# Kernel optimization log

Hardware: AMD Instinct MI355X
Metric: run time of the kernel (lower is better)

## Reference

```python
import jax, jax.numpy as jnp
import numpy as np

NEG_SLOPE = 0.2  # PyG GATConv default


def gat_conv(x, W, a_src, a_dst, b, src, dst, n):
    """Single-head PyG-style GATConv with self-loops already appended to (src, dst)."""
    h = x @ W                                   # [N, F]
    alpha_src = h @ a_src                       # [N]
    alpha_dst = h @ a_dst                       # [N]
    e = alpha_src[src] + alpha_dst[dst]         # [E] per-edge logit (message j->i)
    e = jax.nn.leaky_relu(e, NEG_SLOPE)
    # numerically stable softmax over edges grouped by destination node
    m = jax.ops.segment_max(e, dst, num_segments=n)
    ex = jnp.exp(e - m[dst])
    denom = jax.ops.segment_sum(ex, dst, num_segments=n)
    alpha = ex / denom[dst]                     # [E]
    out = jax.ops.segment_sum(alpha[:, None] * h[src], dst, num_segments=n)
    return out + b


def setup_inputs() -> dict:
    key = jax.random.key(0)
    ks = jax.random.split(key, 16)
    N, C, E = 50000, 128, 800000
    x = jax.random.normal(ks[0], (N, C), dtype=jnp.float32)
    edge_index = jax.random.randint(ks[1], (2, E), 0, N, dtype=jnp.int64)

    def lin(k, din, dout):
        return jax.random.normal(k, (din, dout), dtype=jnp.float32) / np.sqrt(din)

    def att(k, d):
        return jax.random.normal(k, (d,), dtype=jnp.float32) / np.sqrt(d)

    d1, d2, d3 = 2 * C, C // 2, 1
    return {
        "x": x, "edge_index": edge_index,
        "W1": lin(ks[2], C, d1), "as1": att(ks[3], d1), "ad1": att(ks[4], d1), "b1": jnp.zeros((d1,), jnp.float32),
        "W2": lin(ks[5], d1, d2), "as2": att(ks[6], d2), "ad2": att(ks[7], d2), "b2": jnp.zeros((d2,), jnp.float32),
        "W3": lin(ks[8], d2, d3), "as3": att(ks[9], d3), "ad3": att(ks[10], d3), "b3": jnp.zeros((d3,), jnp.float32),
    }


def reference(x, edge_index, W1, as1, ad1, b1, W2, as2, ad2, b2, W3, as3, ad3, b3):
    n = x.shape[0]
    self_loops = jnp.arange(n, dtype=edge_index.dtype)
    src = jnp.concatenate([edge_index[0], self_loops])
    dst = jnp.concatenate([edge_index[1], self_loops])
    # dropout is identity in eval mode
    h = gat_conv(x, W1, as1, ad1, b1, src, dst, n)
    h = jax.nn.elu(h)
    h = gat_conv(h, W2, as2, ad2, b2, src, dst, n)
    h = jax.nn.elu(h)
    return gat_conv(h, W3, as3, ad3, b3, src, dst, n)
```

## Files before the change

### kernel.cpp

```cpp
#include <hip/hip_runtime.h>
#include <hip/hip_bf16.h>
#include <hip/hip_fp16.h>
#include <math.h>

#define NEG_SLOPE 0.2f

typedef __attribute__((ext_vector_type(8))) short bf16x8_t;
typedef __attribute__((ext_vector_type(4))) float f32x4_t;

struct __align__(8) half4_t { __half2 a, b; };

__global__ void hist_k(const int* __restrict__ ei, int E, int n, int* __restrict__ deg) {
    int e = blockIdx.x * 256 + threadIdx.x;
    int ET = E + n;
    if (e >= ET) return;
    int d = (e < E) ? ei[E + e] : (e - E);
    atomicAdd(&deg[d], 1);
}

__global__ void scan1_k(const int* __restrict__ deg, int* __restrict__ incl,
                        int* __restrict__ bsums, int n) {
    __shared__ int s[256];
    int tid = threadIdx.x;
    int i = blockIdx.x * 256 + tid;
    int v = (i < n) ? deg[i] : 0;
    s[tid] = v;
    __syncthreads();
    for (int off = 1; off < 256; off <<= 1) {
        int t = (tid >= off) ? s[tid - off] : 0;
        __syncthreads();
        s[tid] += t;
        __syncthreads();
    }
    if (i < n) incl[i] = s[tid];
    if (tid == 255) bsums[blockIdx.x] = s[255];
}

__global__ void scan2_k(int* __restrict__ bsums, int nch) {
    __shared__ int s[256];
    int tid = threadIdx.x;
    int v = (tid < nch) ? bsums[tid] : 0;
    int orig = v;
    s[tid] = v;
    __syncthreads();
    for (int off = 1; off < 256; off <<= 1) {
        int t = (tid >= off) ? s[tid - off] : 0;
        __syncthreads();
        s[tid] += t;
        __syncthreads();
    }
    if (tid < nch) bsums[tid] = s[tid] - orig;
}

__global__ void scan3_k(int* __restrict__ offsets, int* __restrict__ cursor,
                        const int* __restrict__ bsums, int n, int total) {
    int i = blockIdx.x * 256 + threadIdx.x;
    if (i < n) {
        int excl = offsets[i] - cursor[i] + bsums[i >> 8];
        offsets[i] = excl;
        cursor[i]  = excl;
    }
    if (i == 0 && blockIdx.x == 0) offsets[n] = total;
}

__global__ void fill_k(const int* __restrict__ ei, int E, int n,
                       int* __restrict__ cursor, int* __restrict__ csr) {
    int e = blockIdx.x * 256 + threadIdx.x;
    int ET = E + n;
    if (e >= ET) return;
    int s, d;
    if (e < E) { s = ei[e]; d = ei[E + e]; }
    else       { s = e - E; d = e - E; }
    int pos = atomicAdd(&cursor[d], 1);
    csr[pos] = s;
}

__device__ inline void bf16_split(float f, ushort& hi, ushort& lo) {
    unsigned int u = __float_as_uint(f);
    unsigned int r = u + 0x7FFFu + ((u >> 16) & 1u);
    hi = (ushort)(r >> 16);
    float back = __uint_as_float((unsigned int)hi << 16);
    float rem = f - back;
    unsigned int u2 = __float_as_uint(rem);
    unsigned int r2 = u2 + 0x7FFFu + ((u2 >> 16) & 1u);
    lo = (ushort)(r2 >> 16);
}

__global__ __launch_bounds__(256) void gemm_split_k(const float* __restrict__ A,
                                                    const float* __restrict__ B,
                                                    float* __restrict__ C,
                                                    __half* __restrict__ Ch,
                                                    int M, int K, int Nc) {
    __shared__ __align__(16) ushort sAh[128][40];
    __shared__ __align__(16) ushort sAl[128][40];
    __shared__ __align__(16) ushort sBh[64][40];
    __shared__ __align__(16) ushort sBl[64][40];

    const int tid  = threadIdx.x;
    const int lane = tid & 63;
    const int wv   = tid >> 6;
    const int wm   = wv & 1, wn = wv >> 1;
    const int m0   = blockIdx.x << 7;
    const int n0   = blockIdx.y << 6;

    f32x4_t acc[4][2];
#pragma unroll
    for (int i = 0; i < 4; i++)
#pragma unroll
        for (int j = 0; j < 2; j++) acc[i][j] = (f32x4_t){0.f, 0.f, 0.f, 0.f};

    const int arow = tid >> 1;
    const int acb  = (tid & 1) << 4;
    const int bcol = tid & 63;
    const int bkb  = (tid >> 6) << 3;

    for (int k0 = 0; k0 < K; k0 += 32) {
        {
            float fv[16];
            const int gr = m0 + arow;
            if (gr < M) {
                const float* ap = A + (size_t)gr * K + k0 + acb;
#pragma unroll
                for (int q = 0; q < 4; q++) {
                    float4 t = *(const float4*)(ap + (q << 2));
                    fv[q * 4 + 0] = t.x; fv[q * 4 + 1] = t.y;
                    fv[q * 4 + 2] = t.z; fv[q * 4 + 3] = t.w;
                }
            } else {
#pragma unroll
                for (int q = 0; q < 16; q++) fv[q] = 0.f;
            }
            ushort hv[16], lv[16];
#pragma unroll
            for (int q = 0; q < 16; q++) bf16_split(fv[q], hv[q], lv[q]);
            *(bf16x8_t*)&sAh[arow][acb]     = *(bf16x8_t*)&hv[0];
            *(bf16x8_t*)&sAh[arow][acb + 8] = *(bf16x8_t*)&hv[8];
            *(bf16x8_t*)&sAl[arow][acb]     = *(bf16x8_t*)&lv[0];
            *(bf16x8_t*)&sAl[arow][acb + 8] = *(bf16x8_t*)&lv[8];
        }
        {
            float fv[8];
#pragma unroll
            for (int j = 0; j < 8; j++)
                fv[j] = B[(size_t)(k0 + bkb + j) * Nc + n0 + bcol];
            ushort hv[8], lv[8];
#pragma unroll
            for (int j = 0; j < 8; j++) bf16_split(fv[j], hv[j], lv[j]);
            *(bf16x8_t*)&sBh[bcol][bkb] = *(bf16x8_t*)&hv[0];
            *(bf16x8_t*)&sBl[bcol][bkb] = *(bf16x8_t*)&lv[0];
        }
        __syncthreads();
        bf16x8_t ah[4], al[4], bh[2], bl[2];
        const int rbase = (wm << 6) + (lane & 15);
        const int slot  = (lane >> 4) << 3;
#pragma unroll
        for (int mi = 0; mi < 4; mi++) {
            ah[mi] = *(const bf16x8_t*)&sAh[rbase + (mi << 4)][slot];
            al[mi] = *(const bf16x8_t*)&sAl[rbase + (mi << 4)][slot];
        }
        const int cbase = (wn << 5) + (lane & 15);
#pragma unroll
        for (int ni = 0; ni < 2; ni++) {
            bh[ni] = *(const bf16x8_t*)&sBh[cbase + (ni << 4)][slot];
            bl[ni] = *(const bf16x8_t*)&sBl[cbase + (ni << 4)][slot];
        }
#pragma unroll
        for (int mi = 0; mi < 4; mi++)
#pragma unroll
            for (int ni = 0; ni < 2; ni++) {
                acc[mi][ni] = __builtin_amdgcn_mfma_f32_16x16x32_bf16(ah[mi], bh[ni], acc[mi][ni], 0, 0, 0);
                acc[mi][ni] = __builtin_amdgcn_mfma_f32_16x16x32_bf16(ah[mi], bl[ni], acc[mi][ni], 0, 0, 0);
                acc[mi][ni] = __builtin_amdgcn_mfma_f32_16x16x32_bf16(al[mi], bh[ni], acc[mi][ni], 0, 0, 0);
            }
        __syncthreads();
    }
#pragma unroll
    for (int mi = 0; mi < 4; mi++)
#pragma unroll
        for (int ni = 0; ni < 2; ni++) {
            int row = m0 + (wm << 6) + (mi << 4) + ((lane >> 4) << 2);
            int col = n0 + (wn << 5) + (ni << 4) + (lane & 15);
#pragma unroll
            for (int r = 0; r < 4; r++) {
                if (row + r < M) {
                    float v = acc[mi][ni][r];
                    C[(size_t)(row + r) * Nc + col]  = v;
                    Ch[(size_t)(row + r) * Nc + col] = __float2half(v);
                }
            }
        }
}

template <int D>
__global__ void prep_k(const float* __restrict__ h, const float* __restrict__ avs,
                       const float* __restrict__ avd, float* __restrict__ as_o,
                       float* __restrict__ ad_o, int n) {
    int wid = (blockIdx.x << 2) + (threadIdx.x >> 6);
    int lane = threadIdx.x & 63;
    if (wid >= n) return;
    const float* row = h + (size_t)wid * D;
    float s = 0.f, d = 0.f;
#pragma unroll
    for (int u = 0; u < D / 64; u++) {
        float hv = row[u * 64 + lane];
        s = fmaf(hv, avs[u * 64 + lane], s);
        d = fmaf(hv, avd[u * 64 + lane], d);
    }
#pragma unroll
    for (int o = 32; o; o >>= 1) {
        s += __shfl_xor(s, o);
        d += __shfl_xor(d, o);
    }
    if (lane == 0) { as_o[wid] = s; ad_o[wid] = d; }
}

#define DEG_CAP 128

template <int D, bool DO_ELU>
__global__ __launch_bounds__(256) void agg_k(const int* __restrict__ offs,
                                             const int* __restrict__ csr,
                                             const float* __restrict__ asb,
                                             const float* __restrict__ adb,
                                             const __half* __restrict__ h,
                                             const float* __restrict__ bias,
                                             float* __restrict__ out, int n) {
    __shared__ float wsh[4][DEG_CAP];
    __shared__ int   jsh[4][DEG_CAP];
    const int wv   = threadIdx.x >> 6;
    const int lane = threadIdx.x & 63;
    const int wid  = (blockIdx.x << 2) + wv;
    const bool active = wid < n;

    int beg = 0, deg = 0;
    float adi = 0.f;
    if (active) {
        beg = offs[wid];
        deg = offs[wid + 1] - beg;
        adi = adb[wid];
    }
    const int degc = deg < DEG_CAP ? deg : DEG_CAP;

    float m = -INFINITY;
    if (active) {
        for (int e = lane; e < degc; e += 64) {
            int j = csr[beg + e];
            float v = asb[j] + adi;
            v = v > 0.f ? v : NEG_SLOPE * v;
            jsh[wv][e] = j;
            wsh[wv][e] = v;
            m = fmaxf(m, v);
        }
        for (int e = DEG_CAP + lane; e < deg; e += 64) {
            float v = asb[csr[beg + e]] + adi;
            v = v > 0.f ? v : NEG_SLOPE * v;
            m = fmaxf(m, v);
        }
#pragma unroll
        for (int o = 32; o; o >>= 1) m = fmaxf(m, __shfl_xor(m, o));
    }

    float inv = 0.f;
    if (active) {
        float ssum = 0.f;
        for (int e = lane; e < degc; e += 64) {
            float ww = __expf(wsh[wv][e] - m);
            wsh[wv][e] = ww;
            ssum += ww;
        }
        for (int e = DEG_CAP + lane; e < deg; e += 64) {
            float v = asb[csr[beg + e]] + adi;
            v = v > 0.f ? v : NEG_SLOPE * v;
            ssum += __expf(v - m);
        }
#pragma unroll
        for (int o = 32; o; o >>= 1) ssum += __shfl_xor(ssum, o);
        inv = 1.f / ssum;
    }

    __syncthreads();

    if (!active) return;

    constexpr int U = D / 64;
    float a0[U] = {}, a1[U] = {}, a2[U] = {}, a3[U] = {};

    int e = 0;
    for (; e + 4 <= degc; e += 4) {
        int j0 = jsh[wv][e], j1 = jsh[wv][e + 1], j2 = jsh[wv][e + 2], j3 = jsh[wv][e + 3];
        float w0 = wsh[wv][e], w1 = wsh[wv][e + 1], w2 = wsh[wv][e + 2], w3 = wsh[wv][e + 3];
        if constexpr (U == 4) {
            const half4_t h0 = *(const half4_t*)(h + (size_t)j0 * D + (lane << 2));
            const half4_t h1 = *(const half4_t*)(h + (size_t)j1 * D + (lane << 2));
            const half4_t h2 = *(const half4_t*)(h + (size_t)j2 * D + (lane << 2));
            const half4_t h3 = *(const half4_t*)(h + (size_t)j3 * D + (lane << 2));
            float2 f0a = __half22float2(h0.a), f0b = __half22float2(h0.b);
            float2 f1a = __half22float2(h1.a), f1b = __half22float2(h1.b);
            float2 f2a = __half22float2(h2.a), f2b = __half22float2(h2.b);
            float2 f3a = __half22float2(h3.a), f3b = __half22float2(h3.b);
            a0[0] = fmaf(w0, f0a.x, a0[0]); a0[1] = fmaf(w0, f0a.y, a0[1]);
            a0[2] = fmaf(w0, f0b.x, a0[2]); a0[3] = fmaf(w0, f0b.y, a0[3]);
            a1[0] = fmaf(w1, f1a.x, a1[0]); a1[1] = fmaf(w1, f1a.y, a1[1]);
            a1[2] = fmaf(w1, f1b.x, a1[2]); a1[3] = fmaf(w1, f1b.y, a1[3]);
            a2[0] = fmaf(w2, f2a.x, a2[0]); a2[1] = fmaf(w2, f2a.y, a2[1]);
            a2[2] = fmaf(w2, f2b.x, a2[2]); a2[3] = fmaf(w2, f2b.y, a2[3]);
            a3[0] = fmaf(w3, f3a.x, a3[0]); a3[1] = fmaf(w3, f3a.y, a3[1]);
            a3[2] = fmaf(w3, f3b.x, a3[2]); a3[3] = fmaf(w3, f3b.y, a3[3]);
        } else {
            a0[0] = fmaf(w0, __half2float(h[(size_t)j0 * D + lane]), a0[0]);
            a1[0] = fmaf(w1, __half2float(h[(size_t)j1 * D + lane]), a1[0]);
            a2[0] = fmaf(w2, __half2float(h[(size_t)j2 * D + lane]), a2[0]);
            a3[0] = fmaf(w3, __half2float(h[(size_t)j3 * D + lane]), a3[0]);
        }
    }
    for (; e < degc; ++e) {
        int j = jsh[wv][e];
        float ww = wsh[wv][e];
        if constexpr (U == 4) {
            const half4_t hv = *(const half4_t*)(h + (size_t)j * D + (lane << 2));
            float2 fa = __half22float2(hv.a), fb = __half22float2(hv.b);
            a0[0] = fmaf(ww, fa.x, a0[0]); a0[1] = fmaf(ww, fa.y, a0[1]);
            a0[2] = fmaf(ww, fb.x, a0[2]); a0[3] = fmaf(ww, fb.y, a0[3]);
        } else {
            a0[0] = fmaf(ww, __half2float(h[(size_t)j * D + lane]), a0[0]);
        }
    }
    for (int eo = DEG_CAP; eo < deg; ++eo) {
        int j = csr[beg + eo];
        float v = asb[j] + adi;
        v = v > 0.f ? v : NEG_SLOPE * v;
        float ww = __expf(v - m);
        if constexpr (U == 4) {
            const half4_t hv = *(const half4_t*)(h + (size_t)j * D + (lane << 2));
            float2 fa = __half22float2(hv.a), fb = __half22float2(hv.b);
            a0[0] = fmaf(ww, fa.x, a0[0]); a0[1] = fmaf(ww, fa.y, a0[1]);
            a0[2] = fmaf(ww, fb.x, a0[2]); a0[3] = fmaf(ww, fb.y, a0[3]);
        } else {
            a0[0] = fmaf(ww, __half2float(h[(size_t)j * D + lane]), a0[0]);
        }
    }

    if constexpr (U == 4) {
        float4 o;
        float* po = &o.x;
#pragma unroll
        for (int u = 0; u < 4; u++) {
            float t = (a0[u] + a1[u] + a2[u] + a3[u]) * inv + bias[(lane << 2) + u];
            if (DO_ELU) t = t > 0.f ? t : expm1f(t);
            po[u] = t;
        }
        *(float4*)(out + (size_t)wid * D + (lane << 2)) = o;
    } else {
        float t = (a0[0] + a1[0] + a2[0] + a3[0]) * inv + bias[lane];
        if (DO_ELU) t = t > 0.f ? t : expm1f(t);
        out[(size_t)wid * D + lane] = t;
    }
}

__global__ void l3_prep_k(const float* __restrict__ o2, const float* __restrict__ W3,
                          const float* __restrict__ as3, const float* __restrict__ ad3,
                          float* __restrict__ h3, float* __restrict__ asb,
                          float* __restrict__ adb, int n) {
    int wid = (blockIdx.x << 2) + (threadIdx.x >> 6);
    int lane = threadIdx.x & 63;
    if (wid >= n) return;
    float t = o2[(size_t)wid * 64 + lane] * W3[lane];
#pragma unroll
    for (int o = 32; o; o >>= 1) t += __shfl_xor(t, o);
    if (lane == 0) {
        h3[wid]  = t;
        asb[wid] = t * as3[0];
        adb[wid] = t * ad3[0];
    }
}

__global__ void agg3_k(const int* __restrict__ offs, const int* __restrict__ csr,
                       const float* __restrict__ asb, const float* __restrict__ adb,
                       const float* __restrict__ h3, const float* __restrict__ b3,
                       float* __restrict__ out, int n) {
    int wid = (blockIdx.x << 2) + (threadIdx.x >> 6);
    int lane = threadIdx.x & 63;
    if (wid >= n) return;
    int beg = offs[wid], end = offs[wid + 1];
    float adi = adb[wid];

    float m = -INFINITY;
    for (int e = beg + lane; e < end; e += 64) {
        float v = asb[csr[e]] + adi;
        v = v > 0.f ? v : NEG_SLOPE * v;
        m = fmaxf(m, v);
    }
#pragma unroll
    for (int o = 32; o; o >>= 1) m = fmaxf(m, __shfl_xor(m, o));

    float ssum = 0.f, acc = 0.f;
    for (int e = beg + lane; e < end; e += 64) {
        int j = csr[e];
        float v = asb[j] + adi;
        v = v > 0.f ? v : NEG_SLOPE * v;
        float w = __expf(v - m);
        ssum += w;
        acc = fmaf(w, h3[j], acc);
    }
#pragma unroll
    for (int o = 32; o; o >>= 1) {
        ssum += __shfl_xor(ssum, o);
        acc  += __shfl_xor(acc, o);
    }
    if (lane == 0) out[wid] = acc / ssum + b3[0];
}

extern "C" void kernel_launch(void* const* d_in, const int* in_sizes, int n_in,
                              void* d_out, int out_size, void* d_ws, size_t ws_size,
                              hipStream_t stream) {
    const float* x   = (const float*)d_in[0];
    const int*   ei  = (const int*)d_in[1];
    const float* W1  = (const float*)d_in[2];
    const float* as1 = (const float*)d_in[3];
    const float* ad1 = (const float*)d_in[4];
    const float* b1  = (const float*)d_in[5];
    const float* W2  = (const float*)d_in[6];
    const float* as2 = (const float*)d_in[7];
    const float* ad2 = (const float*)d_in[8];
    const float* b2  = (const float*)d_in[9];
    const float* W3  = (const float*)d_in[10];
    const float* as3 = (const float*)d_in[11];
    const float* ad3 = (const float*)d_in[12];
    const float* b3  = (const float*)d_in[13];

    const int d1 = in_sizes[3];
    const int C  = in_sizes[2] / d1;
    const int N  = in_sizes[0] / C;
    const int E  = in_sizes[1] / 2;
    const int d2 = in_sizes[7];
    const int ET = E + N;

    char* p = (char*)d_ws;
    auto alloc = [&](size_t bytes) -> void* {
        void* q = (void*)p;
        p += (bytes + 255) & ~(size_t)255;
        return q;
    };
    int*    offsets = (int*)alloc(sizeof(int) * (size_t)(N + 1));
    int*    cursor  = (int*)alloc(sizeof(int) * (size_t)N);
    int*    bsums   = (int*)alloc(sizeof(int) * 256);
    int*    csr     = (int*)alloc(sizeof(int) * (size_t)ET);
    float*  asb     = (float*)alloc(sizeof(float) * (size_t)N);
    float*  adb     = (float*)alloc(sizeof(float) * (size_t)N);
    float*  hbuf    = (float*)alloc(sizeof(float) * (size_t)N * d1);
    float*  obuf    = (float*)alloc(sizeof(float) * (size_t)N * d1);
    __half* hhalf   = (__half*)alloc(sizeof(__half) * (size_t)N * d1);

    const int eb  = (ET + 255) / 256;
    const int nch = (N + 255) / 256;
    const int wb  = (N + 3) / 4;

    hipMemsetAsync(cursor, 0, sizeof(int) * (size_t)N, stream);
    hist_k<<<eb, 256, 0, stream>>>(ei, E, N, cursor);
    scan1_k<<<nch, 256, 0, stream>>>(cursor, offsets, bsums, N);
    scan2_k<<<1, 256, 0, stream>>>(bsums, nch);
    scan3_k<<<nch, 256, 0, stream>>>(offsets, cursor, bsums, N, ET);
    fill_k<<<eb, 256, 0, stream>>>(ei, E, N, cursor, csr);

    {
        dim3 g((N + 127) / 128, d1 / 64);
        gemm_split_k<<<g, 256, 0, stream>>>(x, W1, hbuf, hhalf, N, C, d1);
        prep_k<256><<<wb, 256, 0, stream>>>(hbuf, as1, ad1, asb, adb, N);
        agg_k<256, true><<<wb, 256, 0, stream>>>(offsets, csr, asb, adb, hhalf, b1, obuf, N);
    }
    {
        dim3 g((N + 127) / 128, d2 / 64);
        gemm_split_k<<<g, 256, 0, stream>>>(obuf, W2, hbuf, hhalf, N, d1, d2);
        prep_k<64><<<wb, 256, 0, stream>>>(hbuf, as2, ad2, asb, adb, N);
        agg_k<64, true><<<wb, 256, 0, stream>>>(offsets, csr, asb, adb, hhalf, b2, obuf, N);
    }
    {
        l3_prep_k<<<wb, 256, 0, stream>>>(obuf, W3, as3, ad3, hbuf, asb, adb, N);
        agg3_k<<<wb, 256, 0, stream>>>(offsets, csr, asb, adb, hbuf, b3, (float*)d_out, N);
    }
}
```

Before: 388.5 us.

## Pre-split GEMM operands to bf16 hi/lo and fuse attention-logit dots into GEMM epilogue

Moves the bf16 hi/lo splitting out of the GEMM inner loop. The input x and both weight matrices are split in separate kernels, with the weights stored transposed so B tiles load as contiguous vectors. Layer-1 aggregation writes its output directly as bf16 hi/lo. The separate prep_k pass that re-read the fp32 h is removed: the GEMM epilogue computes the partial alpha_src/alpha_dst dot products, reduces them with shuffles and adds them into zeroed buffers with atomics, and the fp32 h store is dropped. The cost is extra split kernels, an extra x read/write pass, atomic adds in place of plain stores, and a non-deterministic summation order for the logits.

```diff
diff --git a/kernel.cpp b/kernel.cpp
--- a/kernel.cpp
+++ b/kernel.cpp
@@ -86,11 +86,42 @@
     lo = (ushort)(r2 >> 16);
 }
 
-__global__ __launch_bounds__(256) void gemm_split_k(const float* __restrict__ A,
-                                                    const float* __restrict__ B,
-                                                    float* __restrict__ C,
-                                                    __half* __restrict__ Ch,
-                                                    int M, int K, int Nc) {
+__global__ void splitA_k(const float* __restrict__ A, ushort* __restrict__ Ah,
+                         ushort* __restrict__ Al, long total8) {
+    long i = (long)blockIdx.x * 256 + threadIdx.x;
+    if (i >= total8) return;
+    const float* src = A + i * 8;
+    float4 a = *(const float4*)src;
+    float4 b = *(const float4*)(src + 4);
+    float fv[8] = {a.x, a.y, a.z, a.w, b.x, b.y, b.z, b.w};
+    ushort hv[8], lv[8];
+#pragma unroll
+    for (int q = 0; q < 8; q++) bf16_split(fv[q], hv[q], lv[q]);
+    *(bf16x8_t*)(Ah + i * 8) = *(bf16x8_t*)hv;
+    *(bf16x8_t*)(Al + i * 8) = *(bf16x8_t*)lv;
+}
+
+__global__ void splitWT_k(const float* __restrict__ W, ushort* __restrict__ WhT,
+                          ushort* __restrict__ WlT, int K, int N) {
+    int idx = blockIdx.x * 256 + threadIdx.x;
+    if (idx >= K * N) return;
+    int k = idx / N, n = idx - k * N;
+    ushort hi, lo;
+    bf16_split(W[idx], hi, lo);
+    WhT[(size_t)n * K + k] = hi;
+    WlT[(size_t)n * K + k] = lo;
+}
+
+__global__ __launch_bounds__(256) void gemm_k(const ushort* __restrict__ Ah,
+                                              const ushort* __restrict__ Al,
+                                              const ushort* __restrict__ BhT,
+                                              const ushort* __restrict__ BlT,
+                                              __half* __restrict__ Ch,
+                                              float* __restrict__ asb,
+                                              float* __restrict__ adb,
+                                              const float* __restrict__ a_src,
+                                              const float* __restrict__ a_dst,
+                                              int M, int K, int Nc) {
     __shared__ __align__(16) ushort sAh[128][40];
     __shared__ __align__(16) ushort sAl[128][40];
     __shared__ __align__(16) ushort sBh[64][40];
@@ -111,43 +142,33 @@
 
     const int arow = tid >> 1;
     const int acb  = (tid & 1) << 4;
-    const int bcol = tid & 63;
-    const int bkb  = (tid >> 6) << 3;
+    const int brow = tid >> 2;
+    const int bkb  = (tid & 3) << 3;
+
+    const bf16x8_t zv = {};
 
     for (int k0 = 0; k0 < K; k0 += 32) {
         {
-            float fv[16];
             const int gr = m0 + arow;
+            bf16x8_t h0 = zv, h1 = zv, l0 = zv, l1 = zv;
             if (gr < M) {
-                const float* ap = A + (size_t)gr * K + k0 + acb;
-#pragma unroll
-                for (int q = 0; q < 4; q++) {
-                    float4 t = *(const float4*)(ap + (q << 2));
-                    fv[q * 4 + 0] = t.x; fv[q * 4 + 1] = t.y;
-                    fv[q * 4 + 2] = t.z; fv[q * 4 + 3] = t.w;
-                }
-            } else {
-#pragma unroll
-                for (int q = 0; q < 16; q++) fv[q] = 0.f;
+                const ushort* ph = Ah + (size_t)gr * K + k0 + acb;
+                const ushort* pl = Al + (size_t)gr * K + k0 + acb;
+                h0 = *(const bf16x8_t*)ph;
+                h1 = *(const bf16x8_t*)(ph + 8);
+                l0 = *(const bf16x8_t*)pl;
+                l1 = *(const bf16x8_t*)(pl + 8);
             }
-            ushort hv[16], lv[16];
-#pragma unroll
-            for (int q = 0; q < 16; q++) bf16_split(fv[q], hv[q], lv[q]);
-            *(bf16x8_t*)&sAh[arow][acb]     = *(bf16x8_t*)&hv[0];
-            *(bf16x8_t*)&sAh[arow][acb + 8] = *(bf16x8_t*)&hv[8];
-            *(bf16x8_t*)&sAl[arow][acb]     = *(bf16x8_t*)&lv[0];
-            *(bf16x8_t*)&sAl[arow][acb + 8] = *(bf16x8_t*)&lv[8];
+            *(bf16x8_t*)&sAh[arow][acb]     = h0;
+            *(bf16x8_t*)&sAh[arow][acb + 8] = h1;
+            *(bf16x8_t*)&sAl[arow][acb]     = l0;
+            *(bf16x8_t*)&sAl[arow][acb + 8] = l1;
         }
         {
-            float fv[8];
-#pragma unroll
-            for (int j = 0; j < 8; j++)
-                fv[j] = B[(size_t)(k0 + bkb + j) * Nc + n0 + bcol];
-            ushort hv[8], lv[8];
-#pragma unroll
-            for (int j = 0; j < 8; j++) bf16_split(fv[j], hv[j], lv[j]);
-            *(bf16x8_t*)&sBh[bcol][bkb] = *(bf16x8_t*)&hv[0];
-            *(bf16x8_t*)&sBl[bcol][bkb] = *(bf16x8_t*)&lv[0];
+            const ushort* ph = BhT + (size_t)(n0 + brow) * K + k0 + bkb;
+            const ushort* pl = BlT + (size_t)(n0 + brow) * K + k0 + bkb;
+            *(bf16x8_t*)&sBh[brow][bkb] = *(const bf16x8_t*)ph;
+            *(bf16x8_t*)&sBl[brow][bkb] = *(const bf16x8_t*)pl;
         }
         __syncthreads();
         bf16x8_t ah[4], al[4], bh[2], bl[2];
@@ -174,56 +195,59 @@
             }
         __syncthreads();
     }
-#pragma unroll
-    for (int mi = 0; mi < 4; mi++)
+
+    const int col0 = n0 + (wn << 5) + (lane & 15);
+    const float asv0 = a_src[col0],      adv0 = a_dst[col0];
+    const float asv1 = a_src[col0 + 16], adv1 = a_dst[col0 + 16];
+
+#pragma unroll
+    for (int mi = 0; mi < 4; mi++) {
+        const int row0 = m0 + (wm << 6) + (mi << 4) + ((lane >> 4) << 2);
 #pragma unroll
         for (int ni = 0; ni < 2; ni++) {
-            int row = m0 + (wm << 6) + (mi << 4) + ((lane >> 4) << 2);
-            int col = n0 + (wn << 5) + (ni << 4) + (lane & 15);
+            const int col = col0 + (ni << 4);
+#pragma unroll
+            for (int r = 0; r < 4; r++)
+                if (row0 + r < M)
+                    Ch[(size_t)(row0 + r) * Nc + col] = __float2half(acc[mi][ni][r]);
+        }
+        float ss[4], sd[4];
+#pragma unroll
+        for (int r = 0; r < 4; r++) {
+            ss[r] = acc[mi][0][r] * asv0 + acc[mi][1][r] * asv1;
+            sd[r] = acc[mi][0][r] * adv0 + acc[mi][1][r] * adv1;
+        }
+#pragma unroll
+        for (int off = 1; off < 16; off <<= 1) {
 #pragma unroll
             for (int r = 0; r < 4; r++) {
-                if (row + r < M) {
-                    float v = acc[mi][ni][r];
-                    C[(size_t)(row + r) * Nc + col]  = v;
-                    Ch[(size_t)(row + r) * Nc + col] = __float2half(v);
+                ss[r] += __shfl_xor(ss[r], off);
+                sd[r] += __shfl_xor(sd[r], off);
+            }
+        }
+        if ((lane & 15) == 0) {
+#pragma unroll
+            for (int r = 0; r < 4; r++)
+                if (row0 + r < M) {
+                    atomicAdd(&asb[row0 + r], ss[r]);
+                    atomicAdd(&adb[row0 + r], sd[r]);
                 }
-            }
-        }
-}
-
-template <int D>
-__global__ void prep_k(const float* __restrict__ h, const float* __restrict__ avs,
-                       const float* __restrict__ avd, float* __restrict__ as_o,
-                       float* __restrict__ ad_o, int n) {
-    int wid = (blockIdx.x << 2) + (threadIdx.x >> 6);
-    int lane = threadIdx.x & 63;
-    if (wid >= n) return;
-    const float* row = h + (size_t)wid * D;
-    float s = 0.f, d = 0.f;
-#pragma unroll
-    for (int u = 0; u < D / 64; u++) {
-        float hv = row[u * 64 + lane];
-        s = fmaf(hv, avs[u * 64 + lane], s);
-        d = fmaf(hv, avd[u * 64 + lane], d);
-    }
-#pragma unroll
-    for (int o = 32; o; o >>= 1) {
-        s += __shfl_xor(s, o);
-        d += __shfl_xor(d, o);
-    }
-    if (lane == 0) { as_o[wid] = s; ad_o[wid] = d; }
+        }
+    }
 }
 
 #define DEG_CAP 128
 
-template <int D, bool DO_ELU>
+template <int D, bool DO_ELU, bool SPLIT_OUT>
 __global__ __launch_bounds__(256) void agg_k(const int* __restrict__ offs,
                                              const int* __restrict__ csr,
                                              const float* __restrict__ asb,
                                              const float* __restrict__ adb,
                                              const __half* __restrict__ h,
                                              const float* __restrict__ bias,
-                                             float* __restrict__ out, int n) {
+                                             float* __restrict__ out,
+                                             ushort* __restrict__ oh,
+                                             ushort* __restrict__ ol, int n) {
     __shared__ float wsh[4][DEG_CAP];
     __shared__ int   jsh[4][DEG_CAP];
     const int wv   = threadIdx.x >> 6;
@@ -340,15 +364,22 @@
     }
 
     if constexpr (U == 4) {
-        float4 o;
-        float* po = &o.x;
+        float t[4];
 #pragma unroll
         for (int u = 0; u < 4; u++) {
-            float t = (a0[u] + a1[u] + a2[u] + a3[u]) * inv + bias[(lane << 2) + u];
-            if (DO_ELU) t = t > 0.f ? t : expm1f(t);
-            po[u] = t;
-        }
-        *(float4*)(out + (size_t)wid * D + (lane << 2)) = o;
+            float v = (a0[u] + a1[u] + a2[u] + a3[u]) * inv + bias[(lane << 2) + u];
+            if (DO_ELU) v = v > 0.f ? v : expm1f(v);
+            t[u] = v;
+        }
+        if constexpr (SPLIT_OUT) {
+            ushort hv[4], lv[4];
+#pragma unroll
+            for (int u = 0; u < 4; u++) bf16_split(t[u], hv[u], lv[u]);
+            *(ushort4*)(oh + (size_t)wid * D + (lane << 2)) = make_ushort4(hv[0], hv[1], hv[2], hv[3]);
+            *(ushort4*)(ol + (size_t)wid * D + (lane << 2)) = make_ushort4(lv[0], lv[1], lv[2], lv[3]);
+        } else {
+            *(float4*)(out + (size_t)wid * D + (lane << 2)) = make_float4(t[0], t[1], t[2], t[3]);
+        }
     } else {
         float t = (a0[0] + a1[0] + a2[0] + a3[0]) * inv + bias[lane];
         if (DO_ELU) t = t > 0.f ? t : expm1f(t);
@@ -444,17 +475,30 @@
     int*    cursor  = (int*)alloc(sizeof(int) * (size_t)N);
     int*    bsums   = (int*)alloc(sizeof(int) * 256);
     int*    csr     = (int*)alloc(sizeof(int) * (size_t)ET);
-    float*  asb     = (float*)alloc(sizeof(float) * (size_t)N);
-    float*  adb     = (float*)alloc(sizeof(float) * (size_t)N);
-    float*  hbuf    = (float*)alloc(sizeof(float) * (size_t)N * d1);
-    float*  obuf    = (float*)alloc(sizeof(float) * (size_t)N * d1);
-    __half* hhalf   = (__half*)alloc(sizeof(__half) * (size_t)N * d1);
+    float*  alpha   = (float*)alloc(sizeof(float) * (size_t)4 * N);
+    float*  as1b = alpha, *ad1b = alpha + N, *as2b = alpha + 2 * N, *ad2b = alpha + 3 * N;
+    ushort* xh      = (ushort*)alloc(sizeof(ushort) * (size_t)N * C);
+    ushort* xl      = (ushort*)alloc(sizeof(ushort) * (size_t)N * C);
+    ushort* w1h     = (ushort*)alloc(sizeof(ushort) * (size_t)C * d1);
+    ushort* w1l     = (ushort*)alloc(sizeof(ushort) * (size_t)C * d1);
+    ushort* w2h     = (ushort*)alloc(sizeof(ushort) * (size_t)d1 * d2);
+    ushort* w2l     = (ushort*)alloc(sizeof(ushort) * (size_t)d1 * d2);
+    __half* ch1     = (__half*)alloc(sizeof(__half) * (size_t)N * d1);
+    ushort* o1h     = (ushort*)alloc(sizeof(ushort) * (size_t)N * d1);
+    ushort* o1l     = (ushort*)alloc(sizeof(ushort) * (size_t)N * d1);
+    __half* ch2     = (__half*)alloc(sizeof(__half) * (size_t)N * d2);
+    float*  o2      = (float*)alloc(sizeof(float) * (size_t)N * d2);
+    float*  h3      = (float*)alloc(sizeof(float) * (size_t)N);
+    float*  as3b    = (float*)alloc(sizeof(float) * (size_t)N);
+    float*  ad3b    = (float*)alloc(sizeof(float) * (size_t)N);
 
     const int eb  = (ET + 255) / 256;
     const int nch = (N + 255) / 256;
     const int wb  = (N + 3) / 4;
 
     hipMemsetAsync(cursor, 0, sizeof(int) * (size_t)N, stream);
+    hipMemsetAsync(alpha, 0, sizeof(float) * (size_t)4 * N, stream);
+
     hist_k<<<eb, 256, 0, stream>>>(ei, E, N, cursor);
     scan1_k<<<nch, 256, 0, stream>>>(cursor, offsets, bsums, N);
     scan2_k<<<1, 256, 0, stream>>>(bsums, nch);
@@ -462,19 +506,26 @@
     fill_k<<<eb, 256, 0, stream>>>(ei, E, N, cursor, csr);
 
     {
+        long t8 = (long)N * C / 8;
+        splitA_k<<<(int)((t8 + 255) / 256), 256, 0, stream>>>(x, xh, xl, t8);
+        splitWT_k<<<(C * d1 + 255) / 256, 256, 0, stream>>>(W1, w1h, w1l, C, d1);
+        splitWT_k<<<(d1 * d2 + 255) / 256, 256, 0, stream>>>(W2, w2h, w2l, d1, d2);
+    }
+
+    {
         dim3 g((N + 127) / 128, d1 / 64);
-        gemm_split_k<<<g, 256, 0, stream>>>(x, W1, hbuf, hhalf, N, C, d1);
-        prep_k<256><<<wb, 256, 0, stream>>>(hbuf, as1, ad1, asb, adb, N);
-        agg_k<256, true><<<wb, 256, 0, stream>>>(offsets, csr, asb, adb, hhalf, b1, obuf, N);
+        gemm_k<<<g, 256, 0, stream>>>(xh, xl, w1h, w1l, ch1, as1b, ad1b, as1, ad1, N, C, d1);
+        agg_k<256, true, true><<<wb, 256, 0, stream>>>(offsets, csr, as1b, ad1b, ch1, b1,
+                                                       nullptr, o1h, o1l, N);
     }
     {
         dim3 g((N + 127) / 128, d2 / 64);
-        gemm_split_k<<<g, 256, 0, stream>>>(obuf, W2, hbuf, hhalf, N, d1, d2);
-        prep_k<64><<<wb, 256, 0, stream>>>(hbuf, as2, ad2, asb, adb, N);
-        agg_k<64, true><<<wb, 256, 0, stream>>>(offsets, csr, asb, adb, hhalf, b2, obuf, N);
+        gemm_k<<<g, 256, 0, stream>>>(o1h, o1l, w2h, w2l, ch2, as2b, ad2b, as2, ad2, N, d1, d2);
+        agg_k<64, true, false><<<wb, 256, 0, stream>>>(offsets, csr, as2b, ad2b, ch2, b2,
+                                                       o2, nullptr, nullptr, N);
     }
     {
-        l3_prep_k<<<wb, 256, 0, stream>>>(obuf, W3, as3, ad3, hbuf, asb, adb, N);
-        agg3_k<<<wb, 256, 0, stream>>>(offsets, csr, asb, adb, hbuf, b3, (float*)d_out, N);
-    }
-}
+        l3_prep_k<<<wb, 256, 0, stream>>>(o2, W3, as3, ad3, h3, as3b, ad3b, N);
+        agg3_k<<<wb, 256, 0, stream>>>(offsets, csr, as3b, ad3b, h3, b3, (float*)d_out, N);
+    }
+}
```

After: 389.4 us. No clear change (+0.2%).
